# Optimization experiments

Hardware: AMD Instinct MI355X
Metric: run time of the kernel (lower is better)

## Reference

```python
import jax, jax.numpy as jnp
import numpy as np

K = 3
PAD = 1
STRIDE = 1
DIL = 1


def _conv(x, w, b):
    # standard 3x3 conv, NCHW / OIHW
    y = jax.lax.conv_general_dilated(
        x, w, (STRIDE, STRIDE), [(PAD, PAD), (PAD, PAD)],
        rhs_dilation=(DIL, DIL),
        dimension_numbers=('NCHW', 'OIHW', 'NCHW'))
    return y + b[None, :, None, None]


def _deform_conv2d(x, offset, mask, weight, bias):
    # x: [B,C,H,W]; offset: [B,2*KK,Ho,Wo] (y,x interleaved per kernel tap);
    # mask: [B,KK,Ho,Wo]; weight: [Co,C,K,K]; bias: [Co]
    B, C, H, W = x.shape
    KK = K * K
    Ho, Wo = offset.shape[2], offset.shape[3]

    off = offset.reshape(B, KK, 2, Ho, Wo)
    dy, dx = off[:, :, 0], off[:, :, 1]          # [B,KK,Ho,Wo]

    ky, kx = jnp.meshgrid(jnp.arange(K), jnp.arange(K), indexing='ij')
    ky = ky.reshape(KK).astype(x.dtype)
    kx = kx.reshape(KK).astype(x.dtype)
    hs = (jnp.arange(Ho) * STRIDE - PAD).astype(x.dtype)
    ws = (jnp.arange(Wo) * STRIDE - PAD).astype(x.dtype)
    base_y = hs[None, :, None] + (ky * DIL)[:, None, None]   # [KK,Ho,1]
    base_x = ws[None, None, :] + (kx * DIL)[:, None, None]   # [KK,1,Wo]

    py = base_y[None] + dy                        # [B,KK,Ho,Wo] sample rows
    px = base_x[None] + dx                        # sample cols

    y0 = jnp.floor(py)
    x0 = jnp.floor(px)
    ly = py - y0                                  # bilinear fractional weights
    lx = px - x0
    y0i = y0.astype(jnp.int32)
    x0i = x0.astype(jnp.int32)

    flat = x.reshape(B, C, H * W)

    def gather(iy, ix):
        # zero-padded gather at integer locations -> [B,C,KK,Ho,Wo]
        valid = (iy >= 0) & (iy < H) & (ix >= 0) & (ix < W)
        iyc = jnp.clip(iy, 0, H - 1)
        ixc = jnp.clip(ix, 0, W - 1)
        idx = (iyc * W + ixc).reshape(B, 1, KK * Ho * Wo)
        g = jnp.take_along_axis(flat, jnp.broadcast_to(idx, (B, C, KK * Ho * Wo)), axis=2)
        g = g.reshape(B, C, KK, Ho, Wo)
        return g * valid[:, None].astype(x.dtype)

    val = (gather(y0i, x0i) * ((1 - ly) * (1 - lx))[:, None]
           + gather(y0i, x0i + 1) * ((1 - ly) * lx)[:, None]
           + gather(y0i + 1, x0i) * (ly * (1 - lx))[:, None]
           + gather(y0i + 1, x0i + 1) * (ly * lx)[:, None])

    val = val * mask[:, None]                     # DCNv2 modulation

    wr = weight.reshape(weight.shape[0], C, KK)   # [Co,C,KK]
    out = jnp.einsum('bckhw,ock->bohw', val, wr)
    return out + bias[None, :, None, None]


def setup_inputs() -> dict:
    key = jax.random.key(0)
    ks = jax.random.split(key, 7)
    B, C, Co, H, W = 4, 128, 256, 96, 96
    KK = K * K
    x = jax.random.normal(ks[0], (B, C, H, W), dtype=jnp.float32)
    weight = jax.random.normal(ks[1], (Co, C, K, K), dtype=jnp.float32) * 0.03
    bias = jax.random.normal(ks[2], (Co,), dtype=jnp.float32) * 0.01
    offset_w = jax.random.normal(ks[3], (2 * KK, C, K, K), dtype=jnp.float32) * 0.01
    offset_b = jax.random.normal(ks[4], (2 * KK,), dtype=jnp.float32) * 0.01
    mod_w = jax.random.normal(ks[5], (KK, C, K, K), dtype=jnp.float32) * 0.01
    mod_b = jnp.ones((KK,), dtype=jnp.float32)
    return {'x': x, 'weight': weight, 'bias': bias,
            'offset_w': offset_w, 'offset_b': offset_b,
            'mod_w': mod_w, 'mod_b': mod_b}


def reference(x, weight, bias, offset_w, offset_b, mod_w, mod_b):
    offset = _conv(x, offset_w, offset_b)
    mask = jax.nn.sigmoid(_conv(x, mod_w, mod_b))
    return _deform_conv2d(x, offset, mask, weight, bias)
```

## Files before the change

### kernel.cpp

```cpp
#include <hip/hip_runtime.h>
#include <math.h>

#define HH 96
#define WW 96
#define HW 9216
#define CIN 128
#define COUT 256

typedef _Float16 f16;
typedef _Float16 f16x2 __attribute__((ext_vector_type(2)));
typedef _Float16 f16x8 __attribute__((ext_vector_type(8)));
typedef __attribute__((ext_vector_type(4))) float f32x4;

static __device__ __forceinline__ unsigned short f2h(float f) {
  union { f16 h; unsigned short u; } v; v.h = (f16)f; return v.u;
}

__global__ __launch_bounds__(256) void k_prep(const float* __restrict__ x,
                                              const float* __restrict__ offw,
                                              const float* __restrict__ modw,
                                              const float* __restrict__ wgt,
                                              unsigned short* __restrict__ xTh,
                                              unsigned short* __restrict__ wAbF,
                                              unsigned short* __restrict__ wTtF) {
  __shared__ float tile[32][130];
  int bid = blockIdx.x;
  int t = threadIdx.x;
  if (bid < 1152) {
    int wseg = bid % 3, h = (bid / 3) % 96, b = bid / 288;
    int w2 = t & 15;
    int cg = t >> 4;
    const float* xbase = x + ((size_t)h * 96) + wseg * 32 + w2 * 2;
#pragma unroll
    for (int i = 0; i < 8; ++i) {
      int c = cg + 16 * i;
      float2 v = *(const float2*)(xbase + (size_t)(b * 128 + c) * HW);
      tile[w2 * 2][c] = v.x;
      tile[w2 * 2 + 1][c] = v.y;
    }
    __syncthreads();
    int w_out = t >> 3;
    int oct = t & 7;
    unsigned short* op =
        xTh + (((size_t)(b * 96 + h) * 96) + wseg * 32 + w_out) * 128 + oct * 8;
#pragma unroll
    for (int it = 0; it < 2; ++it) {
      union { f16x8 v; f16 h[8]; } r;
#pragma unroll
      for (int j = 0; j < 8; ++j)
        r.h[j] = (f16)tile[w_out][it * 64 + oct * 8 + j];
      *(f16x8*)(op + it * 64) = r.v;
    }
  } else if (bid < 1296) {
    int i = (bid - 1152) * 256 + t;
    if (i < 9 * 2 * 4 * 512) {
      int j = i & 7;
      int l = (i >> 3) & 63;
      int ks = (i >> 9) & 3;
      int ng = i >> 11;
      int kpos = ng >> 1, n16 = ng & 1;
      int n = n16 * 16 + (l & 15);
      int c = ks * 32 + (l >> 4) * 8 + j;
      float v = 0.f;
      if (n < 18) v = offw[n * 1152 + c * 9 + kpos];
      else if (n < 27) v = modw[(n - 18) * 1152 + c * 9 + kpos];
      wAbF[i] = f2h(v);
    }
  } else {
    int i = (bid - 1296) * 256 + t;
    if (i < 9 * 16 * 4 * 512) {
      int j = i & 7;
      int l = (i >> 3) & 63;
      int ks = (i >> 9) & 3;
      int ng = i >> 11;
      int kpos = ng >> 4, n16 = ng & 15;
      int n = n16 * 16 + (l & 15);
      int c = ks * 32 + (l >> 4) * 8 + j;
      wTtF[i] = f2h(wgt[n * 1152 + c * 9 + kpos]);
    }
  }
}

__global__ __launch_bounds__(256) void k_main(const unsigned short* __restrict__ xTh,
                                              const unsigned short* __restrict__ wAbF,
                                              const unsigned short* __restrict__ wTtF,
                                              const float* __restrict__ offb,
                                              const float* __restrict__ modb,
                                              const float* __restrict__ bias,
                                              float* __restrict__ out) {
  __shared__ __align__(16) unsigned short Ab[32 * 136];
  __shared__ float om_lds[27 * 33];
  __shared__ float ez[4 * 1040];

  int t = threadIdx.x;
  int l = t & 63, w = t >> 6;
  int lm = l & 15, lq = l >> 4;
  int raw = blockIdx.x;
  int bid = (raw & 7) * 144 + (raw >> 3);
  int pix0 = bid * 32;
  int b = pix0 / HW;
  int posim0 = pix0 % HW;
  int ibase = b * HW;

  {
    int mh = w & 1, n16o = w >> 1;
    int prow = pix0 + mh * 16 + lm;
    int pimo = prow % HW;
    int hoo = pimo / 96, woo = pimo % 96;
    f32x4 acco = (f32x4){0.f, 0.f, 0.f, 0.f};
    const f16x8 zv = {0, 0, 0, 0, 0, 0, 0, 0};
#pragma unroll 1
    for (int kpos = 0; kpos < 9; ++kpos) {
      int dyr = kpos / 3 - 1, dxr = kpos % 3 - 1;
      bool valid = ((unsigned)(hoo + dyr) < 96u) && ((unsigned)(woo + dxr) < 96u);
      int srow = valid ? (prow + dyr * 96 + dxr) : prow;
      const unsigned short* ap = xTh + (size_t)srow * 128 + lq * 8;
      const unsigned short* bp = wAbF + (size_t)((kpos * 2 + n16o) * 4) * 512 + l * 8;
#pragma unroll
      for (int ks = 0; ks < 4; ++ks) {
        f16x8 af = valid ? *(const f16x8*)(ap + ks * 32) : zv;
        f16x8 bf = *(const f16x8*)(bp + (size_t)ks * 512);
        acco = __builtin_amdgcn_mfma_f32_16x16x32_f16(af, bf, acco, 0, 0, 0);
      }
    }
    int n = n16o * 16 + lm;
    if (n < 27) {
      float bv = (n < 18) ? offb[n] : modb[n - 18];
#pragma unroll
      for (int r = 0; r < 4; ++r) {
        float v = acco[r] + bv;
        if (n >= 18) v = 1.f / (1.f + expf(-v));
        om_lds[n * 33 + mh * 16 + lq * 4 + r] = v;
      }
    }
  }
  __syncthreads();

  int pxo = t >> 3;
  int sc8 = t & 7;
  int pimS = (pix0 + pxo) % HW;
  int hoS = pimS / 96, woS = pimS % 96;

  f32x4 acc[2][4];
#pragma unroll
  for (int i = 0; i < 2; ++i)
#pragma unroll
    for (int j = 0; j < 4; ++j)
      acc[i][j] = (f32x4){0.f, 0.f, 0.f, 0.f};

  for (int kpos = 0; kpos < 9; ++kpos) {
    float dy = om_lds[(2 * kpos) * 33 + pxo];
    float dx = om_lds[(2 * kpos + 1) * 33 + pxo];
    float mk = om_lds[(18 + kpos) * 33 + pxo];
    float py = (float)(hoS - 1 + kpos / 3) + dy;
    float pxf = (float)(woS - 1 + kpos % 3) + dx;
    float fy = floorf(py), fx = floorf(pxf);
    int y0 = (int)fy, x0 = (int)fx;
    float ly = py - fy, lx = pxf - fx;
    float w00 = (1.f - ly) * (1.f - lx), w01 = (1.f - ly) * lx;
    float w10 = ly * (1.f - lx),         w11 = ly * lx;
    bool vy0 = (unsigned)y0 < 96u, vy1 = (unsigned)(y0 + 1) < 96u;
    bool vx0 = (unsigned)x0 < 96u, vx1 = (unsigned)(x0 + 1) < 96u;
    w00 = (vy0 && vx0) ? w00 * mk : 0.f;
    w01 = (vy0 && vx1) ? w01 * mk : 0.f;
    w10 = (vy1 && vx0) ? w10 * mk : 0.f;
    w11 = (vy1 && vx1) ? w11 * mk : 0.f;
    int y0c = min(max(y0, 0), 95), y1c = min(max(y0 + 1, 0), 95);
    int x0c = min(max(x0, 0), 95), x1c = min(max(x0 + 1, 0), 95);
    int ofs[4];
    ofs[0] = (ibase + y0c * 96 + x0c) * 128;
    ofs[1] = (ibase + y0c * 96 + x1c) * 128;
    ofs[2] = (ibase + y1c * 96 + x0c) * 128;
    ofs[3] = (ibase + y1c * 96 + x1c) * 128;
    f16 h00 = (f16)w00, h01 = (f16)w01, h10 = (f16)w10, h11 = (f16)w11;
    f16x2 wp[4];
    wp[0] = (f16x2){h00, h00}; wp[1] = (f16x2){h01, h01};
    wp[2] = (f16x2){h10, h10}; wp[3] = (f16x2){h11, h11};

    uint4 q[4][2];
#pragma unroll
    for (int c = 0; c < 4; ++c)
#pragma unroll
      for (int it = 0; it < 2; ++it)
        q[c][it] = *(const uint4*)(xTh + ofs[c] + (sc8 + 8 * it) * 8);

    __syncthreads();
#pragma unroll
    for (int it = 0; it < 2; ++it) {
      union { uint4 u; f16x2 h[4]; } a0, a1, a2, a3;
      a0.u = q[0][it]; a1.u = q[1][it]; a2.u = q[2][it]; a3.u = q[3][it];
      union { f16x8 v; f16x2 h[4]; } r;
#pragma unroll
      for (int j = 0; j < 4; ++j)
        r.h[j] = a0.h[j] * wp[0] + a1.h[j] * wp[1] + a2.h[j] * wp[2] + a3.h[j] * wp[3];
      *(f16x8*)(Ab + pxo * 136 + (sc8 + 8 * it) * 8) = r.v;
    }
    __syncthreads();

#pragma unroll
    for (int ks = 0; ks < 4; ++ks) {
      f16x8 af[2], bfv[4];
#pragma unroll
      for (int mt = 0; mt < 2; ++mt)
        af[mt] = *(const f16x8*)(Ab + (mt * 16 + lm) * 136 + ks * 32 + lq * 8);
      const unsigned short* bp =
          wTtF + (size_t)((kpos * 16 + w * 4) * 4 + ks) * 512 + l * 8;
#pragma unroll
      for (int nt = 0; nt < 4; ++nt)
        bfv[nt] = *(const f16x8*)(bp + (size_t)nt * 4 * 512);
#pragma unroll
      for (int mt = 0; mt < 2; ++mt)
#pragma unroll
        for (int nt = 0; nt < 4; ++nt)
          acc[mt][nt] = __builtin_amdgcn_mfma_f32_16x16x32_f16(af[mt], bfv[nt], acc[mt][nt], 0, 0, 0);
    }
  }

  float bias_v[4];
#pragma unroll
  for (int nt = 0; nt < 4; ++nt) bias_v[nt] = bias[w * 64 + nt * 16 + lm];
  float* z = ez + w * 1040;
#pragma unroll
  for (int mt = 0; mt < 2; ++mt) {
    __syncthreads();
#pragma unroll
    for (int nt = 0; nt < 4; ++nt)
#pragma unroll
      for (int r = 0; r < 4; ++r)
        z[(lq * 4 + r) * 65 + nt * 16 + lm] = acc[mt][nt][r] + bias_v[nt];
    __syncthreads();
    int pxr = l & 15;
    int nb = l >> 4;
#pragma unroll
    for (int s = 0; s < 16; ++s) {
      int n = nb + 4 * s;
      out[((size_t)(b * COUT + w * 64 + n)) * HW + posim0 + mt * 16 + pxr] = z[pxr * 65 + n];
    }
  }
}

extern "C" void kernel_launch(void* const* d_in, const int* in_sizes, int n_in,
                              void* d_out, int out_size, void* d_ws, size_t ws_size,
                              hipStream_t stream) {
  const float* x      = (const float*)d_in[0];
  const float* weight = (const float*)d_in[1];
  const float* bias   = (const float*)d_in[2];
  const float* offw   = (const float*)d_in[3];
  const float* offb   = (const float*)d_in[4];
  const float* modw   = (const float*)d_in[5];
  const float* modb   = (const float*)d_in[6];
  float* out = (float*)d_out;
  float* ws = (float*)d_ws;

  unsigned short* xTh  = (unsigned short*)ws;
  unsigned short* wTtF = (unsigned short*)(ws + 2359296);
  unsigned short* wAbF = (unsigned short*)(ws + 2359296 + 147456);

  k_prep<<<2448, 256, 0, stream>>>(x, offw, modw, weight, xTh, wAbF, wTtF);
  k_main<<<1152, 256, 0, stream>>>(xTh, wAbF, wTtF, offb, modb, bias, out);
}
```

Measured before the change: 149.8 us.

## Process two kernel taps per phase with double LDS buffers

The main loop now handles two kernel taps per iteration, in five phases instead of nine. Each thread issues the bilinear gather loads for both taps before the first barrier, and each tap's interpolated result goes to its own LDS buffer. This doubles the global loads in flight and roughly halves the number of block-wide barriers. The epilogue staging buffer now reuses the same LDS as the A buffers, which lowers total LDS use. The cost is higher register pressure from holding two taps' worth of gathered data.

```diff
diff --git a/kernel.cpp b/kernel.cpp
--- a/kernel.cpp
+++ b/kernel.cpp
@@ -28,8 +28,7 @@
   int t = threadIdx.x;
   if (bid < 1152) {
     int wseg = bid % 3, h = (bid / 3) % 96, b = bid / 288;
-    int w2 = t & 15;
-    int cg = t >> 4;
+    int w2 = t & 15, cg = t >> 4;
     const float* xbase = x + ((size_t)h * 96) + wseg * 32 + w2 * 2;
 #pragma unroll
     for (int i = 0; i < 8; ++i) {
@@ -39,8 +38,7 @@
       tile[w2 * 2 + 1][c] = v.y;
     }
     __syncthreads();
-    int w_out = t >> 3;
-    int oct = t & 7;
+    int w_out = t >> 3, oct = t & 7;
     unsigned short* op =
         xTh + (((size_t)(b * 96 + h) * 96) + wseg * 32 + w_out) * 128 + oct * 8;
 #pragma unroll
@@ -88,9 +86,12 @@
                                               const float* __restrict__ modb,
                                               const float* __restrict__ bias,
                                               float* __restrict__ out) {
-  __shared__ __align__(16) unsigned short Ab[32 * 136];
+  __shared__ __align__(16) unsigned char smem[2 * 32 * 136 * 2];
   __shared__ float om_lds[27 * 33];
-  __shared__ float ez[4 * 1040];
+
+  unsigned short* AbB[2];
+  AbB[0] = (unsigned short*)smem;
+  AbB[1] = (unsigned short*)(smem + 32 * 136 * 2);
 
   int t = threadIdx.x;
   int l = t & 63, w = t >> 6;
@@ -148,78 +149,99 @@
     for (int j = 0; j < 4; ++j)
       acc[i][j] = (f32x4){0.f, 0.f, 0.f, 0.f};
 
-  for (int kpos = 0; kpos < 9; ++kpos) {
-    float dy = om_lds[(2 * kpos) * 33 + pxo];
-    float dx = om_lds[(2 * kpos + 1) * 33 + pxo];
-    float mk = om_lds[(18 + kpos) * 33 + pxo];
-    float py = (float)(hoS - 1 + kpos / 3) + dy;
-    float pxf = (float)(woS - 1 + kpos % 3) + dx;
-    float fy = floorf(py), fx = floorf(pxf);
-    int y0 = (int)fy, x0 = (int)fx;
-    float ly = py - fy, lx = pxf - fx;
-    float w00 = (1.f - ly) * (1.f - lx), w01 = (1.f - ly) * lx;
-    float w10 = ly * (1.f - lx),         w11 = ly * lx;
-    bool vy0 = (unsigned)y0 < 96u, vy1 = (unsigned)(y0 + 1) < 96u;
-    bool vx0 = (unsigned)x0 < 96u, vx1 = (unsigned)(x0 + 1) < 96u;
-    w00 = (vy0 && vx0) ? w00 * mk : 0.f;
-    w01 = (vy0 && vx1) ? w01 * mk : 0.f;
-    w10 = (vy1 && vx0) ? w10 * mk : 0.f;
-    w11 = (vy1 && vx1) ? w11 * mk : 0.f;
-    int y0c = min(max(y0, 0), 95), y1c = min(max(y0 + 1, 0), 95);
-    int x0c = min(max(x0, 0), 95), x1c = min(max(x0 + 1, 0), 95);
-    int ofs[4];
-    ofs[0] = (ibase + y0c * 96 + x0c) * 128;
-    ofs[1] = (ibase + y0c * 96 + x1c) * 128;
-    ofs[2] = (ibase + y1c * 96 + x0c) * 128;
-    ofs[3] = (ibase + y1c * 96 + x1c) * 128;
-    f16 h00 = (f16)w00, h01 = (f16)w01, h10 = (f16)w10, h11 = (f16)w11;
-    f16x2 wp[4];
-    wp[0] = (f16x2){h00, h00}; wp[1] = (f16x2){h01, h01};
-    wp[2] = (f16x2){h10, h10}; wp[3] = (f16x2){h11, h11};
-
-    uint4 q[4][2];
-#pragma unroll
-    for (int c = 0; c < 4; ++c)
-#pragma unroll
-      for (int it = 0; it < 2; ++it)
-        q[c][it] = *(const uint4*)(xTh + ofs[c] + (sc8 + 8 * it) * 8);
-
-    __syncthreads();
-#pragma unroll
-    for (int it = 0; it < 2; ++it) {
-      union { uint4 u; f16x2 h[4]; } a0, a1, a2, a3;
-      a0.u = q[0][it]; a1.u = q[1][it]; a2.u = q[2][it]; a3.u = q[3][it];
-      union { f16x8 v; f16x2 h[4]; } r;
-#pragma unroll
-      for (int j = 0; j < 4; ++j)
-        r.h[j] = a0.h[j] * wp[0] + a1.h[j] * wp[1] + a2.h[j] * wp[2] + a3.h[j] * wp[3];
-      *(f16x8*)(Ab + pxo * 136 + (sc8 + 8 * it) * 8) = r.v;
-    }
-    __syncthreads();
-
-#pragma unroll
-    for (int ks = 0; ks < 4; ++ks) {
-      f16x8 af[2], bfv[4];
-#pragma unroll
-      for (int mt = 0; mt < 2; ++mt)
-        af[mt] = *(const f16x8*)(Ab + (mt * 16 + lm) * 136 + ks * 32 + lq * 8);
-      const unsigned short* bp =
-          wTtF + (size_t)((kpos * 16 + w * 4) * 4 + ks) * 512 + l * 8;
-#pragma unroll
-      for (int nt = 0; nt < 4; ++nt)
-        bfv[nt] = *(const f16x8*)(bp + (size_t)nt * 4 * 512);
-#pragma unroll
-      for (int mt = 0; mt < 2; ++mt)
+#pragma unroll 1
+  for (int ph = 0; ph < 5; ++ph) {
+    int k0 = ph * 2;
+    bool has2 = (k0 + 1 < 9);
+
+    f16x2 wp[2][4];
+    uint4 q[2][4][2];
+#pragma unroll
+    for (int s = 0; s < 2; ++s) {
+      if (s == 1 && !has2) break;
+      int kp = k0 + s;
+      float dy = om_lds[(2 * kp) * 33 + pxo];
+      float dx = om_lds[(2 * kp + 1) * 33 + pxo];
+      float mk = om_lds[(18 + kp) * 33 + pxo];
+      float py = (float)(hoS - 1 + kp / 3) + dy;
+      float pxf = (float)(woS - 1 + kp % 3) + dx;
+      float fy = floorf(py), fx = floorf(pxf);
+      int y0 = (int)fy, x0 = (int)fx;
+      float ly = py - fy, lx = pxf - fx;
+      float w00 = (1.f - ly) * (1.f - lx), w01 = (1.f - ly) * lx;
+      float w10 = ly * (1.f - lx),         w11 = ly * lx;
+      bool vy0 = (unsigned)y0 < 96u, vy1 = (unsigned)(y0 + 1) < 96u;
+      bool vx0 = (unsigned)x0 < 96u, vx1 = (unsigned)(x0 + 1) < 96u;
+      w00 = (vy0 && vx0) ? w00 * mk : 0.f;
+      w01 = (vy0 && vx1) ? w01 * mk : 0.f;
+      w10 = (vy1 && vx0) ? w10 * mk : 0.f;
+      w11 = (vy1 && vx1) ? w11 * mk : 0.f;
+      int y0c = min(max(y0, 0), 95), y1c = min(max(y0 + 1, 0), 95);
+      int x0c = min(max(x0, 0), 95), x1c = min(max(x0 + 1, 0), 95);
+      int ofs0 = (ibase + y0c * 96 + x0c) * 128;
+      int ofs1 = (ibase + y0c * 96 + x1c) * 128;
+      int ofs2 = (ibase + y1c * 96 + x0c) * 128;
+      int ofs3 = (ibase + y1c * 96 + x1c) * 128;
+      f16 h00 = (f16)w00, h01 = (f16)w01, h10 = (f16)w10, h11 = (f16)w11;
+      wp[s][0] = (f16x2){h00, h00}; wp[s][1] = (f16x2){h01, h01};
+      wp[s][2] = (f16x2){h10, h10}; wp[s][3] = (f16x2){h11, h11};
+#pragma unroll
+      for (int it = 0; it < 2; ++it) {
+        int cc = (sc8 + 8 * it) * 8;
+        q[s][0][it] = *(const uint4*)(xTh + ofs0 + cc);
+        q[s][1][it] = *(const uint4*)(xTh + ofs1 + cc);
+        q[s][2][it] = *(const uint4*)(xTh + ofs2 + cc);
+        q[s][3][it] = *(const uint4*)(xTh + ofs3 + cc);
+      }
+    }
+
+    __syncthreads();
+#pragma unroll
+    for (int s = 0; s < 2; ++s) {
+      if (s == 1 && !has2) break;
+#pragma unroll
+      for (int it = 0; it < 2; ++it) {
+        union { uint4 u; f16x2 h[4]; } a0, a1, a2, a3;
+        a0.u = q[s][0][it]; a1.u = q[s][1][it]; a2.u = q[s][2][it]; a3.u = q[s][3][it];
+        union { f16x8 v; f16x2 h[4]; } r;
+#pragma unroll
+        for (int j = 0; j < 4; ++j)
+          r.h[j] = a0.h[j] * wp[s][0] + a1.h[j] * wp[s][1] +
+                   a2.h[j] * wp[s][2] + a3.h[j] * wp[s][3];
+        *(f16x8*)(AbB[s] + pxo * 136 + (sc8 + 8 * it) * 8) = r.v;
+      }
+    }
+    __syncthreads();
+
+#pragma unroll
+    for (int s = 0; s < 2; ++s) {
+      if (s == 1 && !has2) break;
+      int kp = k0 + s;
+      const unsigned short* buf = AbB[s];
+#pragma unroll
+      for (int ks = 0; ks < 4; ++ks) {
+        f16x8 af[2], bfv[4];
+#pragma unroll
+        for (int mt = 0; mt < 2; ++mt)
+          af[mt] = *(const f16x8*)(buf + (mt * 16 + lm) * 136 + ks * 32 + lq * 8);
+        const unsigned short* bp =
+            wTtF + (size_t)((kp * 16 + w * 4) * 4 + ks) * 512 + l * 8;
 #pragma unroll
         for (int nt = 0; nt < 4; ++nt)
-          acc[mt][nt] = __builtin_amdgcn_mfma_f32_16x16x32_f16(af[mt], bfv[nt], acc[mt][nt], 0, 0, 0);
+          bfv[nt] = *(const f16x8*)(bp + (size_t)nt * 4 * 512);
+#pragma unroll
+        for (int mt = 0; mt < 2; ++mt)
+#pragma unroll
+          for (int nt = 0; nt < 4; ++nt)
+            acc[mt][nt] = __builtin_amdgcn_mfma_f32_16x16x32_f16(af[mt], bfv[nt], acc[mt][nt], 0, 0, 0);
+      }
     }
   }
 
   float bias_v[4];
 #pragma unroll
   for (int nt = 0; nt < 4; ++nt) bias_v[nt] = bias[w * 64 + nt * 16 + lm];
-  float* z = ez + w * 1040;
+  float* z = (float*)smem + w * 1040;
 #pragma unroll
   for (int mt = 0; mt < 2; ++mt) {
     __syncthreads();
```

Result: slower. 158.3 us (+5.7%).
